# Kernel tuning notes

Measured on AMD Instinct MI355X. Metric: run time of the kernel, lower is better.

## Reference

```python
import jax, jax.numpy as jnp
import numpy as np

PRED_LEN = 32          # t_eval = linspace(0, pred_len, pred_len)
MAX_STEPS = 12         # adaptive steps budget per eval interval (masked once done)
ATOL, RTOL = 1e-8, 1e-4
SAFETY, MIN_FAC, MAX_FAC = 0.9, 0.2, 10.0

# Tsit5 (Tsitouras 5(4)) tableau
A21 = 0.161
A31, A32 = -0.008480655492356989, 0.335480655492357
A41, A42, A43 = 2.8971530571054935, -6.359448489975075, 4.3622954328695815
A51, A52, A53, A54 = 5.325864828439257, -11.748883564062828, 7.4955393428898365, -0.09249506636175525
A61, A62, A63, A64, A65 = 5.86145544294642, -12.92096931784711, 8.159367898576159, -0.071584973281401, -0.028269050394068383
B1, B2, B3, B4, B5, B6 = 0.09646076681806523, 0.01, 0.4798896504144996, 1.379008574103742, -3.290069515436081, 2.324710524099774
E1, E2, E3, E4, E5, E6, E7 = (-0.00178001105222577714, -0.0008164344596567469, 0.007880878010261995,
                              -0.1447110071732629, 0.5823571654525552, -0.45808210592918697,
                              0.015151515151515152)


def _rhs(y, beta, gamma, mu, N):
    # y: [B,4] = (S, I, R, D)
    S, I = y[:, 0], y[:, 1]
    inf = beta * S * I / N
    return jnp.stack((-inf, inf - (gamma + mu) * I, gamma * I, mu * I), axis=1)


def _integrate_to(y, dt, t0, t1, beta, gamma, mu, N):
    """Adaptive Tsit5 from t0 to t1 (scalars), batched state y [B,4], per-element dt [B]."""
    Bsz = y.shape[0]

    @jax.checkpoint
    def step(carry, _):
        y, t, dt, done = carry
        h = jnp.maximum(jnp.minimum(dt, t1 - t), 1e-9)   # clamp last step to interval end
        hc = h[:, None]
        k1 = _rhs(y, beta, gamma, mu, N)
        k2 = _rhs(y + hc * (A21 * k1), beta, gamma, mu, N)
        k3 = _rhs(y + hc * (A31 * k1 + A32 * k2), beta, gamma, mu, N)
        k4 = _rhs(y + hc * (A41 * k1 + A42 * k2 + A43 * k3), beta, gamma, mu, N)
        k5 = _rhs(y + hc * (A51 * k1 + A52 * k2 + A53 * k3 + A54 * k4), beta, gamma, mu, N)
        k6 = _rhs(y + hc * (A61 * k1 + A62 * k2 + A63 * k3 + A64 * k4 + A65 * k5), beta, gamma, mu, N)
        y_new = y + hc * (B1 * k1 + B2 * k2 + B3 * k3 + B4 * k4 + B5 * k5 + B6 * k6)
        k7 = _rhs(y_new, beta, gamma, mu, N)
        err = hc * (E1 * k1 + E2 * k2 + E3 * k3 + E4 * k4 + E5 * k5 + E6 * k6 + E7 * k7)
        tol = ATOL + RTOL * jnp.maximum(jnp.abs(y), jnp.abs(y_new))
        enorm = jnp.sqrt(jnp.mean((err / tol) ** 2, axis=1))   # RMS error norm, [B]
        accept = (enorm <= 1.0) & (~done)
        fac = jnp.clip(SAFETY * jnp.where(enorm > 0, enorm, 1e-10) ** (-0.2), MIN_FAC, MAX_FAC)
        t2 = jnp.where(accept, t + h, t)
        y2 = jnp.where(accept[:, None], y_new, y)
        dt2 = jnp.where(done, dt, h * fac)
        done2 = done | (t2 >= t1 - 1e-6)
        return (y2, t2, dt2, done2), None

    t = jnp.full((Bsz,), t0, dtype=y.dtype)
    done = jnp.zeros((Bsz,), dtype=bool)
    (y, t, dt, done), _ = jax.lax.scan(step, (y, t, dt, done), None, length=MAX_STEPS)
    return y, dt


def _forward(x, gp, population):
    beta, gamma, mu = x[:, 0], x[:, 1], x[:, 2]
    N = population
    # initial conditions: I0=100, R0=D0=0, S0 = pop - I0
    S0 = gp[:, 0] - 100.0
    z = jnp.zeros_like(S0)
    y0 = jnp.stack((S0, jnp.full_like(S0, 100.0), z, z), axis=1)  # [B,4]
    t_eval = jnp.linspace(0.0, float(PRED_LEN), PRED_LEN).astype(x.dtype)
    pairs = jnp.stack((t_eval[:-1], t_eval[1:]), axis=1)          # [T-1, 2]

    def outer(carry, t01):
        y, dt = carry
        y, dt = _integrate_to(y, dt, t01[0], t01[1], beta, gamma, mu, N)
        return (y, dt), y

    dt0 = jnp.full((y0.shape[0],), 0.05, dtype=y0.dtype)
    (_, _), ys = jax.lax.scan(outer, (y0, dt0), pairs)            # ys: [T-1, B, 4]
    ys = jnp.concatenate((y0[None], ys), axis=0)                  # [T, B, 4]
    return jnp.transpose(ys, (1, 0, 2))                           # [B, T, 4]


def setup_inputs() -> dict:
    key = jax.random.key(0)
    kb, kg, km, kp = jax.random.split(key, 4)
    B = 65536
    beta = 0.1 + 0.4 * jax.random.uniform(kb, (B,), dtype=jnp.float32)
    gamma = 0.05 + 0.15 * jax.random.uniform(kg, (B,), dtype=jnp.float32)
    mu = 0.001 + 0.009 * jax.random.uniform(km, (B,), dtype=jnp.float32)
    x = jnp.stack((beta, gamma, mu), axis=1)                      # [B,3]
    pop = 1e5 + 9e5 * jax.random.uniform(kp, (B,), dtype=jnp.float32)
    gp = pop[:, None]                                             # [B,1]
    return {"x": x, "gp": gp, "population": pop}


def reference(x, gp, population):
    return _forward(x, gp, population)
```

## Files before the change

kernel.cpp:

```cpp
#include <hip/hip_runtime.h>
#include <math.h>


#define PRED_LEN 32
#define MAX_STEPS 12

#define ATOL 1e-08f
#define RTOL 1e-04f

#define A21 0.161f
#define A31 (-0.008480655492356989f)
#define A32 0.335480655492357f
#define A41 2.8971530571054935f
#define A42 (-6.359448489975075f)
#define A43 4.3622954328695815f
#define A51 5.325864828439257f
#define A52 (-11.748883564062828f)
#define A53 7.4955393428898365f
#define A54 (-0.09249506636175525f)
#define A61 5.86145544294642f
#define A62 (-12.92096931784711f)
#define A63 8.159367898576159f
#define A64 (-0.071584973281401f)
#define A65 (-0.028269050394068383f)
#define B1 0.09646076681806523f
#define B2 0.01f
#define B3 0.4798896504144996f
#define B4 1.379008574103742f
#define B5 (-3.290069515436081f)
#define B6 2.324710524099774f
#define E1 (-0.001780011052225777f)
#define E2 (-0.0008164344596567469f)
#define E3 0.007880878010261995f
#define E4 (-0.1447110071732629f)
#define E5 0.5823571654525552f
#define E6 (-0.45808210592918697f)
#define E7 0.015151515151515152f

__global__ __launch_bounds__(256) void sird_tsit5_kernel(
    const float* __restrict__ x,
    const float* __restrict__ gp,
    const float* __restrict__ pop,
    float* __restrict__ out,
    int B)
{
    int b = blockIdx.x * blockDim.x + threadIdx.x;
    if (b >= B) return;

    const float beta  = x[3 * b + 0];
    const float gamma = x[3 * b + 1];
    const float mu    = x[3 * b + 2];
    const float N     = pop[b];
    const float binvN = beta / N;
    const float gm    = gamma + mu;

    float S = gp[b] - 100.0f;
    float I = 100.0f;
    float R = 0.0f;
    float D = 0.0f;
    float dt = 0.05f;

    float4* o = (float4*)(out + (size_t)b * (PRED_LEN * 4));
    o[0] = make_float4(S, I, R, D);

    for (int seg = 0; seg < PRED_LEN - 1; ++seg) {
        const float t0 = (float)(32.0 * (double)seg / 31.0);
        const float t1 = (float)(32.0 * (double)(seg + 1) / 31.0);
        float t = t0;
        bool done = false;

        for (int s = 0; s < MAX_STEPS && !done; ++s) {
            const float h = fmaxf(fminf(dt, t1 - t), 1e-9f);

            const float inf1 = binvN * S * I;
            const float I1   = I;

            float P = A21 * inf1;
            float Q = A21 * I1;
            float St = fmaf(-h, P, S);
            float It = fmaf(h, fmaf(-gm, Q, P), I);
            const float inf2 = binvN * St * It;
            const float I2   = It;

            P = fmaf(A32, inf2, A31 * inf1);
            Q = fmaf(A32, I2,   A31 * I1);
            St = fmaf(-h, P, S);
            It = fmaf(h, fmaf(-gm, Q, P), I);
            const float inf3 = binvN * St * It;
            const float I3   = It;

            P = fmaf(A43, inf3, fmaf(A42, inf2, A41 * inf1));
            Q = fmaf(A43, I3,   fmaf(A42, I2,   A41 * I1));
            St = fmaf(-h, P, S);
            It = fmaf(h, fmaf(-gm, Q, P), I);
            const float inf4 = binvN * St * It;
            const float I4   = It;

            P = fmaf(A54, inf4, fmaf(A53, inf3, fmaf(A52, inf2, A51 * inf1)));
            Q = fmaf(A54, I4,   fmaf(A53, I3,   fmaf(A52, I2,   A51 * I1)));
            St = fmaf(-h, P, S);
            It = fmaf(h, fmaf(-gm, Q, P), I);
            const float inf5 = binvN * St * It;
            const float I5   = It;

            P = fmaf(A65, inf5, fmaf(A64, inf4, fmaf(A63, inf3, fmaf(A62, inf2, A61 * inf1))));
            Q = fmaf(A65, I5,   fmaf(A64, I4,   fmaf(A63, I3,   fmaf(A62, I2,   A61 * I1))));
            St = fmaf(-h, P, S);
            It = fmaf(h, fmaf(-gm, Q, P), I);
            const float inf6 = binvN * St * It;
            const float I6   = It;

            const float Pb = fmaf(B6, inf6, fmaf(B5, inf5, fmaf(B4, inf4, fmaf(B3, inf3, fmaf(B2, inf2, B1 * inf1)))));
            const float Qb = fmaf(B6, I6,   fmaf(B5, I5,   fmaf(B4, I4,   fmaf(B3, I3,   fmaf(B2, I2,   B1 * I1)))));
            const float hg = h * gamma;
            const float hm = h * mu;
            const float Sn = fmaf(-h, Pb, S);
            const float In = fmaf(h, fmaf(-gm, Qb, Pb), I);
            const float Rn = fmaf(hg, Qb, R);
            const float Dn = fmaf(hm, Qb, D);

            const float inf7 = binvN * Sn * In;
            const float I7   = In;

            const float Pe = fmaf(E7, inf7, fmaf(E6, inf6, fmaf(E5, inf5, fmaf(E4, inf4, fmaf(E3, inf3, fmaf(E2, inf2, E1 * inf1))))));
            const float Qe = fmaf(E7, I7,   fmaf(E6, I6,   fmaf(E5, I5,   fmaf(E4, I4,   fmaf(E3, I3,   fmaf(E2, I2,   E1 * I1))))));
            const float e0 = h * Pe;
            const float e1 = h * fmaf(-gm, Qe, Pe);
            const float e2 = hg * Qe;
            const float e3 = hm * Qe;

            const float tol0 = fmaf(RTOL, fmaxf(fabsf(S), fabsf(Sn)), ATOL);
            const float tol1 = fmaf(RTOL, fmaxf(fabsf(I), fabsf(In)), ATOL);
            const float tol2 = fmaf(RTOL, fmaxf(fabsf(R), fabsf(Rn)), ATOL);
            const float tol3 = fmaf(RTOL, fmaxf(fabsf(D), fabsf(Dn)), ATOL);

            const float r0 = e0 * __builtin_amdgcn_rcpf(tol0);
            const float r1 = e1 * __builtin_amdgcn_rcpf(tol1);
            const float r2 = e2 * __builtin_amdgcn_rcpf(tol2);
            const float r3 = e3 * __builtin_amdgcn_rcpf(tol3);

            float sumsq = r0 * r0;
            sumsq = fmaf(r1, r1, sumsq);
            sumsq = fmaf(r2, r2, sumsq);
            sumsq = fmaf(r3, r3, sumsq);
            const float q = 0.25f * sumsq;

            const bool accept = (q <= 1.0f);
            const float ql  = fmaxf(q, 1e-20f);
            float fac = 0.9f * __builtin_amdgcn_exp2f(-0.1f * __builtin_amdgcn_logf(ql));
            fac = fminf(fmaxf(fac, 0.2f), 10.0f);

            t = accept ? (t + h) : t;
            S = accept ? Sn : S;
            I = accept ? In : I;
            R = accept ? Rn : R;
            D = accept ? Dn : D;
            dt = h * fac;
            done = (t >= t1 - 1e-6f);
        }

        o[seg + 1] = make_float4(S, I, R, D);
    }
}

extern "C" void kernel_launch(void* const* d_in, const int* in_sizes, int n_in,
                              void* d_out, int out_size, void* d_ws, size_t ws_size,
                              hipStream_t stream) {
    const float* x   = (const float*)d_in[0];
    const float* gp  = (const float*)d_in[1];
    const float* pop = (const float*)d_in[2];
    float* out = (float*)d_out;
    const int B = in_sizes[2];

    const int block = 256;
    const int grid = (B + block - 1) / block;
    sird_tsit5_kernel<<<grid, block, 0, stream>>>(x, gp, pop, out, B);
}
```

Measured before the change: 79.22 us.

## Flatten nested segment/step loops and reuse FSAL stage derivative

Merges the per-segment outer loop and the adaptive inner step loop into a single while loop with a step counter, so lanes of a wavefront that finish a segment early move on to the next segment instead of idling until the slowest lane finishes. It also reuses the last stage evaluation (inf7) as the next step's first stage (first-same-as-last), which removes one RHS multiply per step. The cost is more divergent control flow around the segment-advance branch and output store. Products are also reassociated as (binvN*St)*It, which may change rounding slightly.

```diff
diff --git a/kernel.cpp b/kernel.cpp
--- a/kernel.cpp
+++ b/kernel.cpp
@@ -63,103 +63,107 @@
     float4* o = (float4*)(out + (size_t)b * (PRED_LEN * 4));
     o[0] = make_float4(S, I, R, D);
 
-    for (int seg = 0; seg < PRED_LEN - 1; ++seg) {
-        const float t0 = (float)(32.0 * (double)seg / 31.0);
-        const float t1 = (float)(32.0 * (double)(seg + 1) / 31.0);
-        float t = t0;
-        bool done = false;
+    float inf1 = binvN * S * I;
+    float t  = 0.0f;
+    float t1 = (float)(32.0 * 1.0 / 31.0);
+    int seg  = 0;
+    int scnt = 0;
 
-        for (int s = 0; s < MAX_STEPS && !done; ++s) {
-            const float h = fmaxf(fminf(dt, t1 - t), 1e-9f);
+    while (seg < PRED_LEN - 1) {
+        const float h = fmaxf(fminf(dt, t1 - t), 1e-9f);
+        const float I1 = I;
 
-            const float inf1 = binvN * S * I;
-            const float I1   = I;
+        float P = A21 * inf1;
+        float Q = A21 * I1;
+        float St = fmaf(-h, P, S);
+        float It = fmaf(h, fmaf(-gm, Q, P), I);
+        const float inf2 = (binvN * St) * It;
+        const float I2   = It;
 
-            float P = A21 * inf1;
-            float Q = A21 * I1;
-            float St = fmaf(-h, P, S);
-            float It = fmaf(h, fmaf(-gm, Q, P), I);
-            const float inf2 = binvN * St * It;
-            const float I2   = It;
+        P = fmaf(A32, inf2, A31 * inf1);
+        Q = fmaf(A32, I2,   A31 * I1);
+        St = fmaf(-h, P, S);
+        It = fmaf(h, fmaf(-gm, Q, P), I);
+        const float inf3 = (binvN * St) * It;
+        const float I3   = It;
 
-            P = fmaf(A32, inf2, A31 * inf1);
-            Q = fmaf(A32, I2,   A31 * I1);
-            St = fmaf(-h, P, S);
-            It = fmaf(h, fmaf(-gm, Q, P), I);
-            const float inf3 = binvN * St * It;
-            const float I3   = It;
+        P = fmaf(A43, inf3, fmaf(A42, inf2, A41 * inf1));
+        Q = fmaf(A43, I3,   fmaf(A42, I2,   A41 * I1));
+        St = fmaf(-h, P, S);
+        It = fmaf(h, fmaf(-gm, Q, P), I);
+        const float inf4 = (binvN * St) * It;
+        const float I4   = It;
 
-            P = fmaf(A43, inf3, fmaf(A42, inf2, A41 * inf1));
-            Q = fmaf(A43, I3,   fmaf(A42, I2,   A41 * I1));
-            St = fmaf(-h, P, S);
-            It = fmaf(h, fmaf(-gm, Q, P), I);
-            const float inf4 = binvN * St * It;
-            const float I4   = It;
+        P = fmaf(A54, inf4, fmaf(A53, inf3, fmaf(A52, inf2, A51 * inf1)));
+        Q = fmaf(A54, I4,   fmaf(A53, I3,   fmaf(A52, I2,   A51 * I1)));
+        St = fmaf(-h, P, S);
+        It = fmaf(h, fmaf(-gm, Q, P), I);
+        const float inf5 = (binvN * St) * It;
+        const float I5   = It;
 
-            P = fmaf(A54, inf4, fmaf(A53, inf3, fmaf(A52, inf2, A51 * inf1)));
-            Q = fmaf(A54, I4,   fmaf(A53, I3,   fmaf(A52, I2,   A51 * I1)));
-            St = fmaf(-h, P, S);
-            It = fmaf(h, fmaf(-gm, Q, P), I);
-            const float inf5 = binvN * St * It;
-            const float I5   = It;
+        P = fmaf(A65, inf5, fmaf(A64, inf4, fmaf(A63, inf3, fmaf(A62, inf2, A61 * inf1))));
+        Q = fmaf(A65, I5,   fmaf(A64, I4,   fmaf(A63, I3,   fmaf(A62, I2,   A61 * I1))));
+        St = fmaf(-h, P, S);
+        It = fmaf(h, fmaf(-gm, Q, P), I);
+        const float inf6 = (binvN * St) * It;
+        const float I6   = It;
 
-            P = fmaf(A65, inf5, fmaf(A64, inf4, fmaf(A63, inf3, fmaf(A62, inf2, A61 * inf1))));
-            Q = fmaf(A65, I5,   fmaf(A64, I4,   fmaf(A63, I3,   fmaf(A62, I2,   A61 * I1))));
-            St = fmaf(-h, P, S);
-            It = fmaf(h, fmaf(-gm, Q, P), I);
-            const float inf6 = binvN * St * It;
-            const float I6   = It;
+        const float Pb = fmaf(B6, inf6, fmaf(B5, inf5, fmaf(B4, inf4, fmaf(B3, inf3, fmaf(B2, inf2, B1 * inf1)))));
+        const float Qb = fmaf(B6, I6,   fmaf(B5, I5,   fmaf(B4, I4,   fmaf(B3, I3,   fmaf(B2, I2,   B1 * I1)))));
+        const float hg = h * gamma;
+        const float hm = h * mu;
+        const float Sn = fmaf(-h, Pb, S);
+        const float In = fmaf(h, fmaf(-gm, Qb, Pb), I);
+        const float Rn = fmaf(hg, Qb, R);
+        const float Dn = fmaf(hm, Qb, D);
 
-            const float Pb = fmaf(B6, inf6, fmaf(B5, inf5, fmaf(B4, inf4, fmaf(B3, inf3, fmaf(B2, inf2, B1 * inf1)))));
-            const float Qb = fmaf(B6, I6,   fmaf(B5, I5,   fmaf(B4, I4,   fmaf(B3, I3,   fmaf(B2, I2,   B1 * I1)))));
-            const float hg = h * gamma;
-            const float hm = h * mu;
-            const float Sn = fmaf(-h, Pb, S);
-            const float In = fmaf(h, fmaf(-gm, Qb, Pb), I);
-            const float Rn = fmaf(hg, Qb, R);
-            const float Dn = fmaf(hm, Qb, D);
+        const float inf7 = (binvN * Sn) * In;
+        const float I7   = In;
 
-            const float inf7 = binvN * Sn * In;
-            const float I7   = In;
+        const float Pe = fmaf(E7, inf7, fmaf(E6, inf6, fmaf(E5, inf5, fmaf(E4, inf4, fmaf(E3, inf3, fmaf(E2, inf2, E1 * inf1))))));
+        const float Qe = fmaf(E7, I7,   fmaf(E6, I6,   fmaf(E5, I5,   fmaf(E4, I4,   fmaf(E3, I3,   fmaf(E2, I2,   E1 * I1))))));
+        const float e0 = h * Pe;
+        const float e1 = h * fmaf(-gm, Qe, Pe);
+        const float e2 = hg * Qe;
+        const float e3 = hm * Qe;
 
-            const float Pe = fmaf(E7, inf7, fmaf(E6, inf6, fmaf(E5, inf5, fmaf(E4, inf4, fmaf(E3, inf3, fmaf(E2, inf2, E1 * inf1))))));
-            const float Qe = fmaf(E7, I7,   fmaf(E6, I6,   fmaf(E5, I5,   fmaf(E4, I4,   fmaf(E3, I3,   fmaf(E2, I2,   E1 * I1))))));
-            const float e0 = h * Pe;
-            const float e1 = h * fmaf(-gm, Qe, Pe);
-            const float e2 = hg * Qe;
-            const float e3 = hm * Qe;
+        const float tol0 = fmaf(RTOL, fmaxf(fabsf(S), fabsf(Sn)), ATOL);
+        const float tol1 = fmaf(RTOL, fmaxf(fabsf(I), fabsf(In)), ATOL);
+        const float tol2 = fmaf(RTOL, fmaxf(fabsf(R), fabsf(Rn)), ATOL);
+        const float tol3 = fmaf(RTOL, fmaxf(fabsf(D), fabsf(Dn)), ATOL);
 
-            const float tol0 = fmaf(RTOL, fmaxf(fabsf(S), fabsf(Sn)), ATOL);
-            const float tol1 = fmaf(RTOL, fmaxf(fabsf(I), fabsf(In)), ATOL);
-            const float tol2 = fmaf(RTOL, fmaxf(fabsf(R), fabsf(Rn)), ATOL);
-            const float tol3 = fmaf(RTOL, fmaxf(fabsf(D), fabsf(Dn)), ATOL);
+        const float r0 = e0 * __builtin_amdgcn_rcpf(tol0);
+        const float r1 = e1 * __builtin_amdgcn_rcpf(tol1);
+        const float r2 = e2 * __builtin_amdgcn_rcpf(tol2);
+        const float r3 = e3 * __builtin_amdgcn_rcpf(tol3);
 
-            const float r0 = e0 * __builtin_amdgcn_rcpf(tol0);
-            const float r1 = e1 * __builtin_amdgcn_rcpf(tol1);
-            const float r2 = e2 * __builtin_amdgcn_rcpf(tol2);
-            const float r3 = e3 * __builtin_amdgcn_rcpf(tol3);
+        float sumsq = r0 * r0;
+        sumsq = fmaf(r1, r1, sumsq);
+        sumsq = fmaf(r2, r2, sumsq);
+        sumsq = fmaf(r3, r3, sumsq);
+        const float q = 0.25f * sumsq;
 
-            float sumsq = r0 * r0;
-            sumsq = fmaf(r1, r1, sumsq);
-            sumsq = fmaf(r2, r2, sumsq);
-            sumsq = fmaf(r3, r3, sumsq);
-            const float q = 0.25f * sumsq;
+        const float ql = fmaxf(q, 1e-20f);
+        float fac = 0.9f * __builtin_amdgcn_exp2f(-0.1f * __builtin_amdgcn_logf(ql));
+        fac = fminf(fmaxf(fac, 0.2f), 10.0f);
 
-            const bool accept = (q <= 1.0f);
-            const float ql  = fmaxf(q, 1e-20f);
-            float fac = 0.9f * __builtin_amdgcn_exp2f(-0.1f * __builtin_amdgcn_logf(ql));
-            fac = fminf(fmaxf(fac, 0.2f), 10.0f);
+        const bool accept = (q <= 1.0f);
+        t    = accept ? (t + h) : t;
+        S    = accept ? Sn : S;
+        I    = accept ? In : I;
+        R    = accept ? Rn : R;
+        D    = accept ? Dn : D;
+        inf1 = accept ? inf7 : inf1;
+        dt = h * fac;
+        ++scnt;
 
-            t = accept ? (t + h) : t;
-            S = accept ? Sn : S;
-            I = accept ? In : I;
-            R = accept ? Rn : R;
-            D = accept ? Dn : D;
-            dt = h * fac;
-            done = (t >= t1 - 1e-6f);
+        if ((t >= t1 - 1e-6f) || (scnt >= MAX_STEPS)) {
+            o[seg + 1] = make_float4(S, I, R, D);
+            ++seg;
+            scnt = 0;
+            t  = (float)(32.0 * (double)seg / 31.0);
+            t1 = (float)(32.0 * (double)(seg + 1) / 31.0);
         }
-
-        o[seg + 1] = make_float4(S, I, R, D);
     }
 }
 
```

After: 79.12 us. Within noise of the previous version (-0.1%).
